# Kernel optimization log

Measured on AMD Instinct MI355X. Metric: run time of the kernel, lower is better.

The kernel has to match this reference:

```python
import jax, jax.numpy as jnp
import numpy as np
from jax import lax

B = 8192
DEPTH = 4096
SCALES = 3
FLT = 4  # db2 filter length

_DB2_DEC_LO = np.array([-0.12940952255092145, 0.22414386804185735, 0.836516303737469, 0.48296291314469025], dtype=np.float32)
_DB2_DEC_HI = np.array([-0.48296291314469025, 0.836516303737469, 0.22414386804185735, 0.12940952255092145], dtype=np.float32)


def _coeff_lens(depth, flen, scales):
    # mirrors pywt.dwt_coeff_len(n, flen, 'zero') = floor((n + flen - 1) / 2)
    lens = [depth]
    for _ in range(scales):
        lens.append((lens[-1] + flen - 1) // 2)
    lens = lens[1:]
    lens.append(lens[-1])
    return lens  # e.g. [2049, 1026, 514, 514]

WAVE_DEPTH = int(np.sum(_coeff_lens(DEPTH, FLT, SCALES)))  # 4103


def setup_inputs() -> dict:
    key = jax.random.key(0)
    ks = jax.random.split(key, 5)
    x = jax.random.normal(ks[0], (B, DEPTH), dtype=jnp.float32)
    diag_b = 1.0 + 0.1 * jax.random.normal(ks[1], (DEPTH,), dtype=jnp.float32)
    diag_g = 1.0 + 0.1 * jax.random.normal(ks[2], (WAVE_DEPTH,), dtype=jnp.float32)
    diag_s = 1.0 + 0.1 * jax.random.normal(ks[3], (DEPTH,), dtype=jnp.float32)
    dec_lo = jnp.asarray(_DB2_DEC_LO)
    dec_hi = jnp.asarray(_DB2_DEC_HI)
    rec_lo = dec_lo[::-1]
    rec_hi = dec_hi[::-1]
    perm_idx = jax.random.permutation(ks[4], WAVE_DEPTH).astype(jnp.int32)
    return {"x": x, "diag_b": diag_b, "diag_g": diag_g, "diag_s": diag_s,
            "dec_lo": dec_lo, "dec_hi": dec_hi, "rec_lo": rec_lo, "rec_hi": rec_hi,
            "perm_idx": perm_idx}


def _forward(x, diag_b, diag_g, diag_s, dec_lo, dec_hi, rec_lo, rec_hi, perm_idx):
    L = dec_lo.shape[0]
    lens = _coeff_lens(x.shape[-1], L, SCALES)
    # mul_b: diag(vec) matmul == elementwise column scale
    a = x * diag_b
    # multi-level analysis DWT with 'zero' padding: full convolution, keep odd indices
    w_dec = jnp.stack([dec_lo[::-1], dec_hi[::-1]])[:, None, :]  # [2,1,L] (flip: lax does corr)
    details = []
    for _ in range(SCALES):
        y = lax.conv_general_dilated(a[:, None, :], w_dec, (2,), [(L - 2, L - 1)],
                                     dimension_numbers=("NCH", "OIH", "NCH"))
        a, d = y[:, 0, :], y[:, 1, :]
        details.append(d)
    c = jnp.concatenate([a] + details[::-1], axis=-1)  # [B, WAVE_DEPTH], [cA_s, cD_s, ..., cD_1]
    # mul_p: permutation matmul == column gather
    c = c[:, perm_idx]
    # mul_g
    c = c * diag_g
    # coefficient slicing exactly as in the original forward (incl. its start-update rule)
    rev = lens[::-1]
    coeffs = []
    start = 0
    for s_i in range(SCALES + 1):
        stop = start + rev[s_i]
        coeffs.append(c[:, start:stop])
        start = lens[s_i]
    # multi-level reconstruction (idwt, zero mode): zero-upsample, full conv, trim L-2 per side
    a = coeffs[0]
    w_rec = jnp.stack([rec_lo[::-1], rec_hi[::-1]])[None, :, :]  # [1,2,L]
    for d in coeffs[1:]:
        if a.shape[-1] == d.shape[-1] + 1:  # pywt waverec odd-length trim
            a = a[:, :-1]
        xin = jnp.stack([a, d], axis=1)  # [B,2,la]
        a = lax.conv_general_dilated(xin, w_rec, (1,), [(1, 1)], lhs_dilation=(2,),
                                     dimension_numbers=("NCH", "OIH", "NCH"))[:, 0, :]
    # mul_s
    return a * diag_s


def reference(x, diag_b, diag_g, diag_s, dec_lo, dec_hi, rec_lo, rec_hi, perm_idx):
    return _forward(x, diag_b, diag_g, diag_s, dec_lo, dec_hi, rec_lo, rec_hi, perm_idx)
```

## Files before the change

kernel.cpp:

```cpp
#include <hip/hip_runtime.h>


#define NTHREADS 256

__device__ __forceinline__ float getz(const float* b, int t, int N) {
    return ((unsigned)t < (unsigned)N) ? b[t] : 0.0f;
}

__global__ __launch_bounds__(NTHREADS) void wavelet_fused(
    const float* __restrict__ x,
    const float* __restrict__ diag_b,
    const float* __restrict__ diag_g,
    const float* __restrict__ diag_s,
    const float* __restrict__ dec_lo,
    const float* __restrict__ dec_hi,
    const float* __restrict__ rec_lo,
    const float* __restrict__ rec_hi,
    const int*   __restrict__ perm_idx,
    float* __restrict__ out)
{
    __shared__ __align__(16) float P[4104];
    __shared__ __align__(16) float Q[4104];
    __shared__ __align__(16) float R[2052];

    const int tid = threadIdx.x;
    const long row = blockIdx.x;

    const float lo0=dec_lo[0], lo1=dec_lo[1], lo2=dec_lo[2], lo3=dec_lo[3];
    const float hi0=dec_hi[0], hi1=dec_hi[1], hi2=dec_hi[2], hi3=dec_hi[3];
    const float rl0=rec_lo[0], rl1=rec_lo[1], rl2=rec_lo[2], rl3=rec_lo[3];
    const float rh0=rec_hi[0], rh1=rec_hi[1], rh2=rec_hi[2], rh3=rec_hi[3];

    const float4* xr = (const float4*)(x + row * 4096);
    const float4* bb = (const float4*)diag_b;
    float4* P4 = (float4*)P;
    for (int i = tid; i < 1024; i += NTHREADS) {
        float4 v = xr[i], w = bb[i];
        v.x *= w.x; v.y *= w.y; v.z *= w.z; v.w *= w.w;
        P4[i] = v;
    }
    __syncthreads();

    for (int n = tid; n < 2049; n += NTHREADS) {
        float A0 = getz(P, 2*n+1, 4096);
        float A1 = getz(P, 2*n,   4096);
        float A2 = getz(P, 2*n-1, 4096);
        float A3 = getz(P, 2*n-2, 4096);
        R[n]        = lo0*A0 + lo1*A1 + lo2*A2 + lo3*A3;
        Q[2054 + n] = hi0*A0 + hi1*A1 + hi2*A2 + hi3*A3;
    }
    __syncthreads();

    for (int n = tid; n < 1026; n += NTHREADS) {
        float A0 = getz(R, 2*n+1, 2049);
        float A1 = getz(R, 2*n,   2049);
        float A2 = getz(R, 2*n-1, 2049);
        float A3 = getz(R, 2*n-2, 2049);
        P[n]        = lo0*A0 + lo1*A1 + lo2*A2 + lo3*A3;
        Q[1028 + n] = hi0*A0 + hi1*A1 + hi2*A2 + hi3*A3;
    }
    __syncthreads();

    for (int n = tid; n < 514; n += NTHREADS) {
        float A0 = getz(P, 2*n+1, 1026);
        float A1 = getz(P, 2*n,   1026);
        float A2 = getz(P, 2*n-1, 1026);
        float A3 = getz(P, 2*n-2, 1026);
        Q[n]       = lo0*A0 + lo1*A1 + lo2*A2 + lo3*A3;
        Q[514 + n] = hi0*A0 + hi1*A1 + hi2*A2 + hi3*A3;
    }
    __syncthreads();

    for (int i = tid; i < 4103; i += NTHREADS) {
        P[i] = Q[perm_idx[i]] * diag_g[i];
    }
    __syncthreads();

    for (int p = tid; p < 513; p += NTHREADS) {
        float a0 = P[p],        a1 = P[p+1];
        float d0 = P[2049 + p], d1 = P[2049 + p + 1];
        R[2*p]   = rl2*a0 + rl0*a1 + rh2*d0 + rh0*d1;
        R[2*p+1] = rl3*a0 + rl1*a1 + rh3*d0 + rh1*d1;
    }
    __syncthreads();

    for (int p = tid; p < 1025; p += NTHREADS) {
        float a0 = R[p],        a1 = R[p+1];
        float d0 = P[1026 + p], d1 = P[1026 + p + 1];
        Q[2*p]   = rl2*a0 + rl0*a1 + rh2*d0 + rh0*d1;
        Q[2*p+1] = rl3*a0 + rl1*a1 + rh3*d0 + rh1*d1;
    }
    __syncthreads();

    const float4* ss = (const float4*)diag_s;
    float4* outr = (float4*)(out + row * 4096);
    for (int q = tid; q < 1024; q += NTHREADS) {
        int h = 2 * q;
        float a0 = Q[h],       a1 = Q[h+1],       a2 = Q[h+2];
        float d0 = P[514 + h], d1 = P[514 + h+1], d2 = P[514 + h+2];
        float4 s4 = ss[q];
        float4 o;
        o.x = (rl2*a0 + rl0*a1 + rh2*d0 + rh0*d1) * s4.x;
        o.y = (rl3*a0 + rl1*a1 + rh3*d0 + rh1*d1) * s4.y;
        o.z = (rl2*a1 + rl0*a2 + rh2*d1 + rh0*d2) * s4.z;
        o.w = (rl3*a1 + rl1*a2 + rh3*d1 + rh1*d2) * s4.w;
        outr[q] = o;
    }
}

extern "C" void kernel_launch(void* const* d_in, const int* in_sizes, int n_in,
                              void* d_out, int out_size, void* d_ws, size_t ws_size,
                              hipStream_t stream) {
    const float* x       = (const float*)d_in[0];
    const float* diag_b  = (const float*)d_in[1];
    const float* diag_g  = (const float*)d_in[2];
    const float* diag_s  = (const float*)d_in[3];
    const float* dec_lo  = (const float*)d_in[4];
    const float* dec_hi  = (const float*)d_in[5];
    const float* rec_lo  = (const float*)d_in[6];
    const float* rec_hi  = (const float*)d_in[7];
    const int*   perm    = (const int*)d_in[8];
    float* out = (float*)d_out;

    const int B = in_sizes[0] / 4096;
    wavelet_fused<<<B, NTHREADS, 0, stream>>>(
        x, diag_b, diag_g, diag_s, dec_lo, dec_hi, rec_lo, rec_hi, perm, out);
}
```

Baseline: 297.4 us.

## Shrink shared buffers to two arrays and double block size for occupancy

Reworks the shared-memory plan from three buffers (about 40 KB) to two (about 32 KB) by rerouting intermediate DWT and IDWT stages between them, with an extra copy of the level-2 detail coefficients. Threads per block rise from 256 to 512, and the launch bound asks for higher occupancy. Reconstruction stores are paired as float2 writes. The aim is more resident waves per CU to hide global-memory latency, at the cost of an added LDS copy pass and more register pressure.

Result: faster. 261.4 us (-12.1%).

```diff
diff --git a/kernel.cpp b/kernel.cpp
--- a/kernel.cpp
+++ b/kernel.cpp
@@ -1,13 +1,13 @@
 #include <hip/hip_runtime.h>
 
 
-#define NTHREADS 256
+#define NT 512
 
 __device__ __forceinline__ float getz(const float* b, int t, int N) {
     return ((unsigned)t < (unsigned)N) ? b[t] : 0.0f;
 }
 
-__global__ __launch_bounds__(NTHREADS) void wavelet_fused(
+__global__ __launch_bounds__(NT, 8) void wavelet_fused(
     const float* __restrict__ x,
     const float* __restrict__ diag_b,
     const float* __restrict__ diag_g,
@@ -19,9 +19,8 @@
     const int*   __restrict__ perm_idx,
     float* __restrict__ out)
 {
-    __shared__ __align__(16) float P[4104];
-    __shared__ __align__(16) float Q[4104];
-    __shared__ __align__(16) float R[2052];
+    __shared__ __align__(16) float A[4104];
+    __shared__ __align__(16) float C[4104];
 
     const int tid = threadIdx.x;
     const long row = blockIdx.x;
@@ -31,80 +30,97 @@
     const float rl0=rec_lo[0], rl1=rec_lo[1], rl2=rec_lo[2], rl3=rec_lo[3];
     const float rh0=rec_hi[0], rh1=rec_hi[1], rh2=rec_hi[2], rh3=rec_hi[3];
 
-    const float4* xr = (const float4*)(x + row * 4096);
-    const float4* bb = (const float4*)diag_b;
-    float4* P4 = (float4*)P;
-    for (int i = tid; i < 1024; i += NTHREADS) {
-        float4 v = xr[i], w = bb[i];
-        v.x *= w.x; v.y *= w.y; v.z *= w.z; v.w *= w.w;
-        P4[i] = v;
+    {
+        const float4* xr = (const float4*)(x + row * 4096);
+        const float4* bb = (const float4*)diag_b;
+        float4* A4 = (float4*)A;
+        for (int i = tid; i < 1024; i += NT) {
+            float4 v = xr[i], w = bb[i];
+            v.x *= w.x; v.y *= w.y; v.z *= w.z; v.w *= w.w;
+            A4[i] = v;
+        }
     }
     __syncthreads();
 
-    for (int n = tid; n < 2049; n += NTHREADS) {
-        float A0 = getz(P, 2*n+1, 4096);
-        float A1 = getz(P, 2*n,   4096);
-        float A2 = getz(P, 2*n-1, 4096);
-        float A3 = getz(P, 2*n-2, 4096);
-        R[n]        = lo0*A0 + lo1*A1 + lo2*A2 + lo3*A3;
-        Q[2054 + n] = hi0*A0 + hi1*A1 + hi2*A2 + hi3*A3;
+    for (int n = tid; n < 2049; n += NT) {
+        float A0 = getz(A, 2*n+1, 4096);
+        float A1 = getz(A, 2*n,   4096);
+        float A2 = getz(A, 2*n-1, 4096);
+        float A3 = getz(A, 2*n-2, 4096);
+        C[n]        = lo0*A0 + lo1*A1 + lo2*A2 + lo3*A3;
+        C[2054 + n] = hi0*A0 + hi1*A1 + hi2*A2 + hi3*A3;
     }
     __syncthreads();
 
-    for (int n = tid; n < 1026; n += NTHREADS) {
-        float A0 = getz(R, 2*n+1, 2049);
-        float A1 = getz(R, 2*n,   2049);
-        float A2 = getz(R, 2*n-1, 2049);
-        float A3 = getz(R, 2*n-2, 2049);
-        P[n]        = lo0*A0 + lo1*A1 + lo2*A2 + lo3*A3;
-        Q[1028 + n] = hi0*A0 + hi1*A1 + hi2*A2 + hi3*A3;
+    for (int n = tid; n < 1026; n += NT) {
+        float A0 = getz(C, 2*n+1, 2049);
+        float A1 = getz(C, 2*n,   2049);
+        float A2 = getz(C, 2*n-1, 2049);
+        float A3 = getz(C, 2*n-2, 2049);
+        A[n]        = lo0*A0 + lo1*A1 + lo2*A2 + lo3*A3;
+        A[1026 + n] = hi0*A0 + hi1*A1 + hi2*A2 + hi3*A3;
     }
     __syncthreads();
 
-    for (int n = tid; n < 514; n += NTHREADS) {
-        float A0 = getz(P, 2*n+1, 1026);
-        float A1 = getz(P, 2*n,   1026);
-        float A2 = getz(P, 2*n-1, 1026);
-        float A3 = getz(P, 2*n-2, 1026);
-        Q[n]       = lo0*A0 + lo1*A1 + lo2*A2 + lo3*A3;
-        Q[514 + n] = hi0*A0 + hi1*A1 + hi2*A2 + hi3*A3;
+    for (int n = tid; n < 514; n += NT) {
+        float A0 = getz(A, 2*n+1, 1026);
+        float A1 = getz(A, 2*n,   1026);
+        float A2 = getz(A, 2*n-1, 1026);
+        float A3 = getz(A, 2*n-2, 1026);
+        C[n]       = lo0*A0 + lo1*A1 + lo2*A2 + lo3*A3;
+        C[514 + n] = hi0*A0 + hi1*A1 + hi2*A2 + hi3*A3;
+    }
+    for (int j = tid; j < 1026; j += NT) {
+        C[1028 + j] = A[1026 + j];
     }
     __syncthreads();
 
-    for (int i = tid; i < 4103; i += NTHREADS) {
-        P[i] = Q[perm_idx[i]] * diag_g[i];
+    for (int i = tid; i < 4103; i += NT) {
+        A[i] = C[perm_idx[i]] * diag_g[i];
     }
     __syncthreads();
 
-    for (int p = tid; p < 513; p += NTHREADS) {
-        float a0 = P[p],        a1 = P[p+1];
-        float d0 = P[2049 + p], d1 = P[2049 + p + 1];
-        R[2*p]   = rl2*a0 + rl0*a1 + rh2*d0 + rh0*d1;
-        R[2*p+1] = rl3*a0 + rl1*a1 + rh3*d0 + rh1*d1;
+    {
+        float2* C2 = (float2*)C;
+        for (int p = tid; p < 513; p += NT) {
+            float a0 = A[p],        a1 = A[p+1];
+            float d0 = A[2049 + p], d1 = A[2050 + p];
+            float2 w;
+            w.x = rl2*a0 + rl0*a1 + rh2*d0 + rh0*d1;
+            w.y = rl3*a0 + rl1*a1 + rh3*d0 + rh1*d1;
+            C2[p] = w;
+        }
     }
     __syncthreads();
 
-    for (int p = tid; p < 1025; p += NTHREADS) {
-        float a0 = R[p],        a1 = R[p+1];
-        float d0 = P[1026 + p], d1 = P[1026 + p + 1];
-        Q[2*p]   = rl2*a0 + rl0*a1 + rh2*d0 + rh0*d1;
-        Q[2*p+1] = rl3*a0 + rl1*a1 + rh3*d0 + rh1*d1;
+    {
+        float2* R2 = (float2*)(C + 1028);
+        for (int p = tid; p < 1025; p += NT) {
+            float a0 = C[p],        a1 = C[p+1];
+            float d0 = A[1026 + p], d1 = A[1027 + p];
+            float2 w;
+            w.x = rl2*a0 + rl0*a1 + rh2*d0 + rh0*d1;
+            w.y = rl3*a0 + rl1*a1 + rh3*d0 + rh1*d1;
+            R2[p] = w;
+        }
     }
     __syncthreads();
 
-    const float4* ss = (const float4*)diag_s;
-    float4* outr = (float4*)(out + row * 4096);
-    for (int q = tid; q < 1024; q += NTHREADS) {
-        int h = 2 * q;
-        float a0 = Q[h],       a1 = Q[h+1],       a2 = Q[h+2];
-        float d0 = P[514 + h], d1 = P[514 + h+1], d2 = P[514 + h+2];
-        float4 s4 = ss[q];
-        float4 o;
-        o.x = (rl2*a0 + rl0*a1 + rh2*d0 + rh0*d1) * s4.x;
-        o.y = (rl3*a0 + rl1*a1 + rh3*d0 + rh1*d1) * s4.y;
-        o.z = (rl2*a1 + rl0*a2 + rh2*d1 + rh0*d2) * s4.z;
-        o.w = (rl3*a1 + rl1*a2 + rh3*d1 + rh1*d2) * s4.w;
-        outr[q] = o;
+    {
+        const float4* ss = (const float4*)diag_s;
+        float4* outr = (float4*)(out + row * 4096);
+        for (int q = tid; q < 1024; q += NT) {
+            int h = 2 * q;
+            float a0 = C[1028 + h], a1 = C[1029 + h], a2 = C[1030 + h];
+            float d0 = A[514 + h],  d1 = A[515 + h],  d2 = A[516 + h];
+            float4 s4 = ss[q];
+            float4 o;
+            o.x = (rl2*a0 + rl0*a1 + rh2*d0 + rh0*d1) * s4.x;
+            o.y = (rl3*a0 + rl1*a1 + rh3*d0 + rh1*d1) * s4.y;
+            o.z = (rl2*a1 + rl0*a2 + rh2*d1 + rh0*d2) * s4.z;
+            o.w = (rl3*a1 + rl1*a2 + rh3*d1 + rh1*d2) * s4.w;
+            outr[q] = o;
+        }
     }
 }
 
@@ -123,6 +139,6 @@
     float* out = (float*)d_out;
 
     const int B = in_sizes[0] / 4096;
-    wavelet_fused<<<B, NTHREADS, 0, stream>>>(
+    wavelet_fused<<<B, NT, 0, stream>>>(
         x, diag_b, diag_g, diag_s, dec_lo, dec_hi, rec_lo, rec_hi, perm, out);
 }
```
